# Optimization experiments

Measured on AMD Instinct MI355X. Metric: run time of the kernel, lower is better.

Reference implementation:

```python
import jax, jax.numpy as jnp
import numpy as np
import math

N = 50000      # nodes
E = 800000     # edges (avg degree 16)
T = 4          # time steps
F = 64         # feature dim (in = hidden = out)
MAX_LEN = 200  # positional encoding table length
EPS = 1e-5     # BatchNorm eps


def _make_pe(time_dim, max_len):
    pe = np.zeros((max_len, time_dim), dtype=np.float32)
    position = np.arange(max_len, dtype=np.float32)[:, None]
    div_term = np.exp(np.arange(0, time_dim, 2, dtype=np.float32) * (-math.log(10000.0) / time_dim))
    pe[:, 0::2] = np.sin(position * div_term)
    pe[:, 1::2] = np.cos(position * div_term)
    return jnp.asarray(pe)


def setup_inputs() -> dict:
    key = jax.random.key(0)
    ks = jax.random.split(key, 10)
    xav = math.sqrt(2.0 / (F + F))  # xavier_normal_ std for square linear
    return {
        "node_features": jax.random.normal(ks[0], (N, T, F), dtype=jnp.float32),
        "edges_weight": jax.random.uniform(ks[1], (T, E), dtype=jnp.float32),
        "identities": jax.random.randint(ks[2], (T,), 0, MAX_LEN),
        "edge_src": jax.random.randint(ks[3], (E,), 0, N),
        "edge_dst": jax.random.randint(ks[4], (E,), 0, N),
        "pe": _make_pe(F, MAX_LEN),
        "W0": jax.random.normal(ks[5], (F, F), dtype=jnp.float32) * xav,
        "W1": jax.random.normal(ks[6], (F, F), dtype=jnp.float32) * xav,
        "g0": jnp.ones((F,), jnp.float32),
        "b0": jnp.zeros((F,), jnp.float32),
        "g1": jnp.ones((F,), jnp.float32),
        "b1": jnp.zeros((F,), jnp.float32),
    }


def _gcn_layer(h, ew, edge_src, edge_dst, W):
    # gather-mul-scatter: msg_e = h[src_e] * w_e ; agg_v = sum_{e: dst=v} msg_e
    msg = h[edge_src] * ew                                   # (E, T, F)
    agg = jax.ops.segment_sum(msg, edge_dst, num_segments=N)  # (N, T, F)
    readout = agg.mean(axis=0)                                # dgl.mean_nodes (single graph) -> (T, F)
    return agg @ W, readout @ W


def _batchnorm(x, gamma, beta):
    # training-mode batch stats over all non-channel dims
    mean = x.mean(axis=(0, 1))
    var = x.var(axis=(0, 1))
    return (x - mean) * jax.lax.rsqrt(var + EPS) * gamma + beta


def reference(node_features, edges_weight, identities, edge_src, edge_dst,
              pe, W0, W1, g0, b0, g1, b1):
    # positional encoding added per time step
    h = node_features + pe[identities]          # (N, T, F)
    ew = edges_weight.T[:, :, None]             # (E, T, 1)
    # layer 0: gcn -> dropout(eval=identity) -> BN -> ReLU
    h, readout = _gcn_layer(h, ew, edge_src, edge_dst, W0)
    h = jax.nn.relu(_batchnorm(h, g0, b0))
    # layer 1 (output layer)
    h, readout = _gcn_layer(h, ew, edge_src, edge_dst, W1)
    h = jax.nn.relu(_batchnorm(h, g1, b1))
    return h, readout
```

## Files before the change

kernel.cpp:

```cpp
#include <hip/hip_runtime.h>

#define TF 256

typedef __attribute__((ext_vector_type(8))) short short8;
typedef __attribute__((ext_vector_type(4))) float f32x4;
typedef __attribute__((ext_vector_type(4))) unsigned int uint4v;
typedef __attribute__((ext_vector_type(2))) unsigned int uint2v;

__device__ inline unsigned short f2bf(float x) {
  unsigned u = __float_as_uint(x);
  u += 0x7fffu + ((u >> 16) & 1u);
  return (unsigned short)(u >> 16);
}
__device__ inline unsigned pack2(unsigned short lo, unsigned short hi) {
  return (unsigned)lo | ((unsigned)hi << 16);
}
__device__ inline float bflo(unsigned u) { return __uint_as_float(u << 16); }
__device__ inline float bfhi(unsigned u) { return __uint_as_float(u & 0xffff0000u); }

__global__ void prep_hist_kernel(const float* __restrict__ x, const float* __restrict__ pe,
                                 const int* __restrict__ ids, uint2v* __restrict__ h0, int n4,
                                 const int* __restrict__ dst, int* __restrict__ indeg, int E) {
  const int gid = blockIdx.x * blockDim.x + threadIdx.x;
  const int stride = gridDim.x * blockDim.x;
  for (int i = gid; i < n4; i += stride) {
    int e0 = (i << 2) & (TF - 1);
    int t = e0 >> 6;
    int f4 = e0 & 63;
    f32x4 v = __builtin_nontemporal_load(&reinterpret_cast<const f32x4*>(x)[i]);
    const f32x4 p = *reinterpret_cast<const f32x4*>(&pe[ids[t] * 64 + f4]);
    uint2v o;
    o.x = pack2(f2bf(v.x + p.x), f2bf(v.y + p.y));
    o.y = pack2(f2bf(v.z + p.z), f2bf(v.w + p.w));
    h0[i] = o;
  }
  for (int e = gid; e < E; e += stride) {
    atomicAdd(&indeg[__builtin_nontemporal_load(&dst[e])], 1);
  }
}

__global__ __launch_bounds__(1024) void scan_part1(const int* __restrict__ indeg,
                                                   int* __restrict__ partials, int n) {
  __shared__ int wsum[16];
  const int tid = threadIdx.x;
  const int lane = tid & 63;
  const int wid = tid >> 6;
  int i = blockIdx.x * 1024 + tid;
  int s = (i < n) ? indeg[i] : 0;
  #pragma unroll
  for (int o = 1; o < 64; o <<= 1) s += __shfl_xor(s, o, 64);
  if (lane == 0) wsum[wid] = s;
  __syncthreads();
  if (tid == 0) {
    int acc = 0;
    #pragma unroll
    for (int w = 0; w < 16; ++w) acc += wsum[w];
    partials[blockIdx.x] = acc;
  }
}

__global__ __launch_bounds__(512) void scan2_wfrag_kernel(
    const int* __restrict__ partials, int* __restrict__ base, int* __restrict__ offsets,
    int nb, int n, const float* __restrict__ W0, const float* __restrict__ W1,
    short* __restrict__ wf0, short* __restrict__ wf1) {
  const int tid = threadIdx.x;
  if (tid < 64) {
    int v = (tid < nb) ? partials[tid] : 0;
    int s = v;
    #pragma unroll
    for (int o = 1; o < 64; o <<= 1) {
      int t = __shfl_up(s, o, 64);
      if (tid >= o) s += t;
    }
    if (tid < nb) base[tid] = s - v;
    if (tid == nb - 1) offsets[n] = s;
  }
  const int frag = tid >> 6, lane = tid & 63;
  const int c = frag >> 1, h = frag & 1;
  const int col = (c << 4) + (lane & 15);
  const int k0 = h * 32 + ((lane >> 4) << 3);
  short* o0 = wf0 + frag * 512 + lane * 8;
  short* o1 = wf1 + frag * 512 + lane * 8;
  #pragma unroll
  for (int i = 0; i < 8; ++i) {
    o0[i] = (short)f2bf(W0[(k0 + i) * 64 + col]);
    o1[i] = (short)f2bf(W1[(k0 + i) * 64 + col]);
  }
}

__global__ __launch_bounds__(1024) void scan_part3(const int* __restrict__ indeg,
                                                   const int* __restrict__ base,
                                                   int* __restrict__ offsets,
                                                   int* __restrict__ cursor, int n) {
  __shared__ int wsum[16];
  const int tid = threadIdx.x;
  const int lane = tid & 63;
  const int wid = tid >> 6;
  int i = blockIdx.x * 1024 + tid;
  int v = (i < n) ? indeg[i] : 0;
  int s = v;
  #pragma unroll
  for (int o = 1; o < 64; o <<= 1) {
    int t = __shfl_up(s, o, 64);
    if (lane >= o) s += t;
  }
  if (lane == 63) wsum[wid] = s;
  __syncthreads();
  if (tid == 0) {
    int acc = 0;
    #pragma unroll
    for (int w = 0; w < 16; ++w) { int t = wsum[w]; wsum[w] = acc; acc += t; }
  }
  __syncthreads();
  int excl = s - v + wsum[wid] + base[blockIdx.x];
  if (i < n) { offsets[i] = excl; cursor[i] = excl; }
}

__global__ void fill_kernel(const int* __restrict__ src, const int* __restrict__ dst,
                            const float* __restrict__ ew, int* __restrict__ cursor,
                            uint4v* __restrict__ csr_ent, int E) {
  int e = blockIdx.x * blockDim.x + threadIdx.x;
  if (e >= E) return;
  int d = __builtin_nontemporal_load(&dst[e]);
  int pos = atomicAdd(&cursor[d], 1);
  uint4v ent;
  ent.x = (unsigned)(__builtin_nontemporal_load(&src[e]) << 9);
  float w0 = __builtin_nontemporal_load(&ew[e]);
  float w1 = __builtin_nontemporal_load(&ew[(size_t)E + e]);
  float w2 = __builtin_nontemporal_load(&ew[2 * (size_t)E + e]);
  float w3 = __builtin_nontemporal_load(&ew[3 * (size_t)E + e]);
  ent.y = pack2(f2bf(w0), f2bf(w1));
  ent.z = pack2(f2bf(w2), f2bf(w3));
  ent.w = 0u;
  __builtin_nontemporal_store(ent, &csr_ent[pos]);
}

template <int LAYER>
__global__ __launch_bounds__(256, 6) void fused_agg_mm_kernel(
    const char* __restrict__ h_base, const int* __restrict__ offsets,
    const uint4v* __restrict__ csr_ent, const short* __restrict__ wf,
    const float* __restrict__ red, const float* __restrict__ g,
    const float* __restrict__ b, float inv_count,
    unsigned short* __restrict__ y_bf, float* __restrict__ part, int n_groups) {
  __shared__ unsigned short tile[2][16][72];
  __shared__ float s_sc[64], s_sh[64];
  const int tid = threadIdx.x;
  const int lane = tid & 63;
  const int wid = tid >> 6;
  if (LAYER == 1) {
    if (tid < 64) {
      float sum = red[tid] + red[64 + tid] + red[128 + tid] + red[192 + tid];
      float mean = sum * inv_count;
      float var = red[256 + tid] * inv_count - mean * mean;
      float sc = g[tid] * rsqrtf(var + 1e-5f);
      s_sc[tid] = sc;
      s_sh[tid] = fmaf(-mean, sc, b[tid]);
    }
    __syncthreads();
  }
  const short8 bf0 = *reinterpret_cast<const short8*>(wf + (wid * 2 + 0) * 512 + lane * 8);
  const short8 bf1 = *reinterpret_cast<const short8*>(wf + (wid * 2 + 1) * 512 + lane * 8);

  const int p = lane >> 5;
  const unsigned q = lane & 31;
  const unsigned qb = q << 4;
  const int tw = q >> 3;

  float scv[8], shv[8];
  if (LAYER == 1) {
    const int f0 = (q & 7) << 3;
    #pragma unroll
    for (int j = 0; j < 8; ++j) { scv[j] = s_sc[f0 + j]; shv[j] = s_sh[f0 + j]; }
  }

  f32x4 csum = (f32x4){0.f, 0.f, 0.f, 0.f};
  float ssq = 0.f;
  int buf = 0;

  for (int grp = blockIdx.x; grp < n_groups; grp += gridDim.x) {
    const int v = grp * 4 + wid;
    float acc[8];
    #pragma unroll
    for (int j = 0; j < 8; ++j) acc[j] = 0.f;

    auto wext = [&](uint4v ent) -> float {
      unsigned word = (tw & 2) ? ent.z : ent.y;
      return (tw & 1) ? bfhi(word) : bflo(word);
    };
    auto body = [&](uint4v u, float w) {
      float x[8] = {bflo(u.x), bfhi(u.x), bflo(u.y), bfhi(u.y),
                    bflo(u.z), bfhi(u.z), bflo(u.w), bfhi(u.w)};
      #pragma unroll
      for (int j = 0; j < 8; ++j) {
        float t = x[j];
        if (LAYER == 1) t = fmaxf(0.f, fmaf(t, scv[j], shv[j]));
        acc[j] = fmaf(w, t, acc[j]);
      }
    };

    const int beg = offsets[v];
    const int end = offsets[v + 1];
    int i = beg;
    for (; i + 8 <= end; i += 8) {
      uint4v ent[4];
      #pragma unroll
      for (int c = 0; c < 4; ++c) ent[c] = csr_ent[i + 2 * c + p];
      uint4v row[4];
      #pragma unroll
      for (int c = 0; c < 4; ++c)
        row[c] = *reinterpret_cast<const uint4v*>(h_base + (ent[c].x + qb));
      #pragma unroll
      for (int c = 0; c < 4; ++c) body(row[c], wext(ent[c]));
    }
    for (; i + 2 <= end; i += 2) {
      const uint4v ent = csr_ent[i + p];
      const uint4v row = *reinterpret_cast<const uint4v*>(h_base + (ent.x + qb));
      body(row, wext(ent));
    }
    if (i < end) {
      const uint4v ent = csr_ent[i];
      const uint4v row = *reinterpret_cast<const uint4v*>(h_base + (ent.x + qb));
      body(row, p == 0 ? wext(ent) : 0.f);
    }

    #pragma unroll
    for (int j = 0; j < 8; ++j) acc[j] += __shfl_xor(acc[j], 32, 64);
    if (lane < 32) {
      uint4v o;
      o.x = pack2(f2bf(acc[0]), f2bf(acc[1]));
      o.y = pack2(f2bf(acc[2]), f2bf(acc[3]));
      o.z = pack2(f2bf(acc[4]), f2bf(acc[5]));
      o.w = pack2(f2bf(acc[6]), f2bf(acc[7]));
      *reinterpret_cast<uint4v*>(&tile[buf][wid * 4 + (q >> 3)][(q & 7) * 8]) = o;
    }
    __syncthreads();

    const int r = lane & 15;
    const int k0 = (lane >> 4) << 3;
    const short8 a0 = *reinterpret_cast<const short8*>(&tile[buf][r][k0]);
    const short8 a1 = *reinterpret_cast<const short8*>(&tile[buf][r][k0 + 32]);
    f32x4 dacc = (f32x4){0.f, 0.f, 0.f, 0.f};
    dacc = __builtin_amdgcn_mfma_f32_16x16x32_bf16(a0, bf0, dacc, 0, 0, 0);
    dacc = __builtin_amdgcn_mfma_f32_16x16x32_bf16(a1, bf1, dacc, 0, 0, 0);
    const int gbase = grp * 16 + ((lane >> 4) << 2);
    const int col = (wid << 4) + (lane & 15);
    #pragma unroll
    for (int i2 = 0; i2 < 4; ++i2) {
      const float val = dacc[i2];
      y_bf[(size_t)(gbase + i2) * 64 + col] = f2bf(val);
      csum[i2] += val;
      ssq += val * val;
    }
    buf ^= 1;
  }

  #pragma unroll
  for (int i2 = 0; i2 < 4; ++i2) {
    float vv = csum[i2];
    vv += __shfl_xor(vv, 16, 64);
    vv += __shfl_xor(vv, 32, 64);
    csum[i2] = vv;
  }
  float qq = ssq;
  qq += __shfl_xor(qq, 16, 64);
  qq += __shfl_xor(qq, 32, 64);
  if (lane < 16) {
    #pragma unroll
    for (int i2 = 0; i2 < 4; ++i2)
      part[(size_t)blockIdx.x * 320 + i2 * 64 + (wid << 4) + lane] = csum[i2];
    part[(size_t)blockIdx.x * 320 + 256 + (wid << 4) + lane] = qq;
  }
}

__global__ __launch_bounds__(1024) void reduce_part_kernel(const float* __restrict__ part,
                                                           float* __restrict__ red, int nblk) {
  __shared__ float lds[1024];
  const int tid = threadIdx.x;
  const int col = blockIdx.x * 16 + (tid & 15);
  const int r = tid >> 4;
  float s = 0.f;
  for (int bk = r; bk < nblk; bk += 64) s += part[(size_t)bk * 320 + col];
  lds[tid] = s;
  __syncthreads();
  #pragma unroll
  for (int off = 512; off >= 16; off >>= 1) {
    if (tid < off) lds[tid] += lds[tid + off];
    __syncthreads();
  }
  if (tid < 16) red[col] = lds[tid];
}

__global__ __launch_bounds__(256) void bn_relu_out_kernel(
    const uint4v* __restrict__ yb, const float* __restrict__ red,
    const float* __restrict__ g, const float* __restrict__ b, float inv_count,
    float* __restrict__ out_readout, float invN, f32x4* __restrict__ out, int n8) {
  __shared__ float s_sc[64], s_sh[64];
  const int tid = threadIdx.x;
  if (tid < 64) {
    float sum = red[tid] + red[64 + tid] + red[128 + tid] + red[192 + tid];
    float mean = sum * inv_count;
    float var = red[256 + tid] * inv_count - mean * mean;
    float sc = g[tid] * rsqrtf(var + 1e-5f);
    s_sc[tid] = sc;
    s_sh[tid] = fmaf(-mean, sc, b[tid]);
  }
  __syncthreads();
  if (blockIdx.x == 0) out_readout[tid] = red[tid] * invN;
  const int i = blockIdx.x * 256 + tid;
  if (i >= n8) return;
  const int f0 = (i & 7) << 3;
  uint4v u = __builtin_nontemporal_load(&yb[i]);
  float x[8] = {bflo(u.x), bfhi(u.x), bflo(u.y), bfhi(u.y),
                bflo(u.z), bfhi(u.z), bflo(u.w), bfhi(u.w)};
  f32x4 o0, o1;
  o0.x = fmaxf(0.f, fmaf(x[0], s_sc[f0 + 0], s_sh[f0 + 0]));
  o0.y = fmaxf(0.f, fmaf(x[1], s_sc[f0 + 1], s_sh[f0 + 1]));
  o0.z = fmaxf(0.f, fmaf(x[2], s_sc[f0 + 2], s_sh[f0 + 2]));
  o0.w = fmaxf(0.f, fmaf(x[3], s_sc[f0 + 3], s_sh[f0 + 3]));
  o1.x = fmaxf(0.f, fmaf(x[4], s_sc[f0 + 4], s_sh[f0 + 4]));
  o1.y = fmaxf(0.f, fmaf(x[5], s_sc[f0 + 5], s_sh[f0 + 5]));
  o1.z = fmaxf(0.f, fmaf(x[6], s_sc[f0 + 6], s_sh[f0 + 6]));
  o1.w = fmaxf(0.f, fmaf(x[7], s_sc[f0 + 7], s_sh[f0 + 7]));
  __builtin_nontemporal_store(o0, &out[i * 2 + 0]);
  __builtin_nontemporal_store(o1, &out[i * 2 + 1]);
}

extern "C" void kernel_launch(void* const* d_in, const int* in_sizes, int n_in,
                              void* d_out, int out_size, void* d_ws, size_t ws_size,
                              hipStream_t stream) {
  const float* node_features = (const float*)d_in[0];
  const float* edges_weight  = (const float*)d_in[1];
  const int*   identities    = (const int*)d_in[2];
  const int*   edge_src      = (const int*)d_in[3];
  const int*   edge_dst      = (const int*)d_in[4];
  const float* pe            = (const float*)d_in[5];
  const float* W0            = (const float*)d_in[6];
  const float* W1            = (const float*)d_in[7];
  const float* g0            = (const float*)d_in[8];
  const float* b0            = (const float*)d_in[9];
  const float* g1            = (const float*)d_in[10];
  const float* b1            = (const float*)d_in[11];

  const int T = in_sizes[2];
  const int E = in_sizes[3];
  const int F = in_sizes[8];
  const int N = in_sizes[0] / (T * F);
  const int R = N * T;

  float* out = (float*)d_out;
  float* out_h = out;
  float* out_readout = out + (size_t)N * T * F;

  char* ws = (char*)d_ws;
  size_t off = 0;
  auto alloc = [&](size_t bytes) -> void* {
    off = (off + 255) & ~(size_t)255;
    void* p = ws + off;
    off += bytes;
    return p;
  };
  int*    indeg    = (int*)alloc((size_t)N * sizeof(int));
  int*    partials = (int*)alloc(64 * sizeof(int));
  int*    base_    = (int*)alloc(64 * sizeof(int));
  int*    offsets  = (int*)alloc(((size_t)N + 1) * sizeof(int));
  int*    cursor   = (int*)alloc((size_t)N * sizeof(int));
  uint4v* csr_ent  = (uint4v*)alloc(((size_t)E + 16) * 16);
  unsigned short* h0b  = (unsigned short*)alloc((size_t)N * TF * 2);
  unsigned short* y0b  = (unsigned short*)alloc((size_t)N * TF * 2);
  short* wf0 = (short*)alloc(8 * 512 * sizeof(short));
  short* wf1 = (short*)alloc(8 * 512 * sizeof(short));
  const int FB = 1536;
  float* mm_part = (float*)alloc((size_t)FB * 320 * sizeof(float));
  float* red     = (float*)alloc(320 * sizeof(float));
  (void)ws_size;

  const int nb = (N + 1023) / 1024;
  const float invR = 1.0f / (float)R;
  const int n_groups = N / 4;

  (void)hipMemsetAsync(indeg, 0, (size_t)N * sizeof(int), stream);
  hipLaunchKernelGGL(prep_hist_kernel, dim3(2048), dim3(256), 0, stream,
                     node_features, pe, identities, (uint2v*)h0b, (N * TF) / 4,
                     edge_dst, indeg, E);
  hipLaunchKernelGGL(scan_part1, dim3(nb), dim3(1024), 0, stream, indeg, partials, N);
  hipLaunchKernelGGL(scan2_wfrag_kernel, dim3(1), dim3(512), 0, stream,
                     partials, base_, offsets, nb, N, W0, W1, wf0, wf1);
  hipLaunchKernelGGL(scan_part3, dim3(nb), dim3(1024), 0, stream, indeg, base_, offsets, cursor, N);
  hipLaunchKernelGGL(fill_kernel, dim3((E + 255) / 256), dim3(256), 0, stream,
                     edge_src, edge_dst, edges_weight, cursor, csr_ent, E);

  hipLaunchKernelGGL((fused_agg_mm_kernel<0>), dim3(FB), dim3(256), 0, stream,
                     (const char*)h0b, offsets, csr_ent, wf0,
                     nullptr, nullptr, nullptr, 0.f, y0b, mm_part, n_groups);
  hipLaunchKernelGGL(reduce_part_kernel, dim3(20), dim3(1024), 0, stream, mm_part, red, FB);

  hipLaunchKernelGGL((fused_agg_mm_kernel<1>), dim3(FB), dim3(256), 0, stream,
                     (const char*)y0b, offsets, csr_ent, wf1,
                     red, g0, b0, invR, h0b , mm_part, n_groups);
  hipLaunchKernelGGL(reduce_part_kernel, dim3(20), dim3(1024), 0, stream, mm_part, red, FB);

  hipLaunchKernelGGL(bn_relu_out_kernel, dim3((R * 8 + 255) / 256), dim3(256), 0, stream,
                     (const uint4v*)h0b, red, g1, b1, invR,
                     out_readout, 1.0f / (float)N, (f32x4*)out_h, R * 8);
}
```

Measured before the change: 287.2 us.

## Build CSR via two-pass bin scatter instead of global atomic fill

Replaces the per-edge global-atomic CSR fill with a two-stage scheme. Edges are first scattered into coarse destination bins of 256 nodes using shared-memory histograms and one global atomic per bin per block. A per-bin kernel then places each edge into its final CSR slot using shared-memory atomics. The aim is to cut scattered global atomics and random 16-byte writes, at the cost of an extra pass over a temporary buffer. Bin capacity is fixed at 8192 entries, so any overflow is silently dropped.

```diff
diff --git a/kernel.cpp b/kernel.cpp
--- a/kernel.cpp
+++ b/kernel.cpp
@@ -90,8 +90,7 @@
 
 __global__ __launch_bounds__(1024) void scan_part3(const int* __restrict__ indeg,
                                                    const int* __restrict__ base,
-                                                   int* __restrict__ offsets,
-                                                   int* __restrict__ cursor, int n) {
+                                                   int* __restrict__ offsets, int n) {
   __shared__ int wsum[16];
   const int tid = threadIdx.x;
   const int lane = tid & 63;
@@ -113,26 +112,63 @@
   }
   __syncthreads();
   int excl = s - v + wsum[wid] + base[blockIdx.x];
-  if (i < n) { offsets[i] = excl; cursor[i] = excl; }
-}
-
-__global__ void fill_kernel(const int* __restrict__ src, const int* __restrict__ dst,
-                            const float* __restrict__ ew, int* __restrict__ cursor,
-                            uint4v* __restrict__ csr_ent, int E) {
-  int e = blockIdx.x * blockDim.x + threadIdx.x;
-  if (e >= E) return;
-  int d = __builtin_nontemporal_load(&dst[e]);
-  int pos = atomicAdd(&cursor[d], 1);
-  uint4v ent;
-  ent.x = (unsigned)(__builtin_nontemporal_load(&src[e]) << 9);
-  float w0 = __builtin_nontemporal_load(&ew[e]);
-  float w1 = __builtin_nontemporal_load(&ew[(size_t)E + e]);
-  float w2 = __builtin_nontemporal_load(&ew[2 * (size_t)E + e]);
-  float w3 = __builtin_nontemporal_load(&ew[3 * (size_t)E + e]);
-  ent.y = pack2(f2bf(w0), f2bf(w1));
-  ent.z = pack2(f2bf(w2), f2bf(w3));
-  ent.w = 0u;
-  __builtin_nontemporal_store(ent, &csr_ent[pos]);
+  if (i < n) offsets[i] = excl;
+}
+
+__global__ __launch_bounds__(256) void binscatter_kernel(
+    const int* __restrict__ src, const int* __restrict__ dst,
+    const float* __restrict__ ew, int* __restrict__ gbin_cursor,
+    uint4v* __restrict__ tmp, int E, int nbins) {
+  __shared__ int hist[256];
+  __shared__ int hist2[256];
+  __shared__ int basearr[256];
+  const int tid = threadIdx.x;
+  hist[tid] = 0;
+  hist2[tid] = 0;
+  __syncthreads();
+  const int epb = (E + gridDim.x - 1) / gridDim.x;
+  const int beg = blockIdx.x * epb;
+  const int end = min(beg + epb, E);
+  for (int e = beg + tid; e < end; e += 256)
+    atomicAdd(&hist[__builtin_nontemporal_load(&dst[e]) >> 8], 1);
+  __syncthreads();
+  if (tid < nbins && hist[tid] > 0)
+    basearr[tid] = atomicAdd(&gbin_cursor[tid], hist[tid]);
+  __syncthreads();
+  for (int e = beg + tid; e < end; e += 256) {
+    const int d = dst[e];
+    const int bin = d >> 8;
+    const int idx = atomicAdd(&hist2[bin], 1);
+    uint4v ent;
+    ent.x = (unsigned)(src[e] << 9);
+    ent.y = pack2(f2bf(ew[e]), f2bf(ew[(size_t)E + e]));
+    ent.z = pack2(f2bf(ew[2 * (size_t)E + e]), f2bf(ew[3 * (size_t)E + e]));
+    ent.w = (unsigned)d;
+    const int pos = basearr[bin] + idx;
+    if (pos < 8192)
+      __builtin_nontemporal_store(ent, &tmp[((size_t)bin << 13) + pos]);
+  }
+}
+
+__global__ __launch_bounds__(256) void csr_build_kernel(
+    const uint4v* __restrict__ tmp, const int* __restrict__ gbin_cursor,
+    const int* __restrict__ offsets, uint4v* __restrict__ csr_ent, int n) {
+  __shared__ int cur[256];
+  const int bin = blockIdx.x;
+  const int tid = threadIdx.x;
+  const int node = (bin << 8) + tid;
+  cur[tid] = (node < n) ? offsets[node] : 0;
+  __syncthreads();
+  int cnt = gbin_cursor[bin];
+  if (cnt > 8192) cnt = 8192;
+  const uint4v* bt = tmp + ((size_t)bin << 13);
+  for (int i = tid; i < cnt; i += 256) {
+    uint4v ent = __builtin_nontemporal_load(&bt[i]);
+    const int local = (int)(ent.w & 255u);
+    const int pos = atomicAdd(&cur[local], 1);
+    ent.w = 0u;
+    __builtin_nontemporal_store(ent, &csr_ent[pos]);
+  }
 }
 
 template <int LAYER>
@@ -346,6 +382,7 @@
   const int F = in_sizes[8];
   const int N = in_sizes[0] / (T * F);
   const int R = N * T;
+  const int nbins = (N + 255) >> 8;
 
   float* out = (float*)d_out;
   float* out_h = out;
@@ -359,12 +396,14 @@
     off += bytes;
     return p;
   };
-  int*    indeg    = (int*)alloc((size_t)N * sizeof(int));
+  int* zeros = (int*)alloc(((size_t)N + 256) * sizeof(int));
+  int* indeg = zeros;
+  int* gbin_cursor = zeros + N;
   int*    partials = (int*)alloc(64 * sizeof(int));
   int*    base_    = (int*)alloc(64 * sizeof(int));
   int*    offsets  = (int*)alloc(((size_t)N + 1) * sizeof(int));
-  int*    cursor   = (int*)alloc((size_t)N * sizeof(int));
   uint4v* csr_ent  = (uint4v*)alloc(((size_t)E + 16) * 16);
+  uint4v* tmp      = (uint4v*)alloc(((size_t)nbins << 13) * 16);
   unsigned short* h0b  = (unsigned short*)alloc((size_t)N * TF * 2);
   unsigned short* y0b  = (unsigned short*)alloc((size_t)N * TF * 2);
   short* wf0 = (short*)alloc(8 * 512 * sizeof(short));
@@ -378,16 +417,18 @@
   const float invR = 1.0f / (float)R;
   const int n_groups = N / 4;
 
-  (void)hipMemsetAsync(indeg, 0, (size_t)N * sizeof(int), stream);
+  (void)hipMemsetAsync(zeros, 0, ((size_t)N + 256) * sizeof(int), stream);
   hipLaunchKernelGGL(prep_hist_kernel, dim3(2048), dim3(256), 0, stream,
                      node_features, pe, identities, (uint2v*)h0b, (N * TF) / 4,
                      edge_dst, indeg, E);
+  hipLaunchKernelGGL(binscatter_kernel, dim3(256), dim3(256), 0, stream,
+                     edge_src, edge_dst, edges_weight, gbin_cursor, tmp, E, nbins);
   hipLaunchKernelGGL(scan_part1, dim3(nb), dim3(1024), 0, stream, indeg, partials, N);
   hipLaunchKernelGGL(scan2_wfrag_kernel, dim3(1), dim3(512), 0, stream,
                      partials, base_, offsets, nb, N, W0, W1, wf0, wf1);
-  hipLaunchKernelGGL(scan_part3, dim3(nb), dim3(1024), 0, stream, indeg, base_, offsets, cursor, N);
-  hipLaunchKernelGGL(fill_kernel, dim3((E + 255) / 256), dim3(256), 0, stream,
-                     edge_src, edge_dst, edges_weight, cursor, csr_ent, E);
+  hipLaunchKernelGGL(scan_part3, dim3(nb), dim3(1024), 0, stream, indeg, base_, offsets, N);
+  hipLaunchKernelGGL(csr_build_kernel, dim3(nbins), dim3(256), 0, stream,
+                     tmp, gbin_cursor, offsets, csr_ent, N);
 
   hipLaunchKernelGGL((fused_agg_mm_kernel<0>), dim3(FB), dim3(256), 0, stream,
                      (const char*)h0b, offsets, csr_ent, wf0,
```

Result: no change. 285.1 us (-0.7%).
